# Optimization experiments

Hardware: AMD Instinct MI355X
Metric: run time of the kernel (lower is better)

The kernel has to match this reference:

```python
import jax, jax.numpy as jnp
import numpy as np

D = 2048
H = 16
HD = D // H
B = 2
T = 2048
EPS = 1e-6


def setup_inputs() -> dict:
    key = jax.random.key(0)
    ks = jax.random.split(key, 12)
    s = lambda fan_in: 1.0 / np.sqrt(fan_in)
    inp = {
        "x": jax.random.normal(ks[0], (B, T, D), dtype=jnp.float32),
        "mask": jnp.tril(jnp.ones((T, T), dtype=jnp.int32))[None, None],  # [1,1,T,T] causal
        "w_norm1": jnp.ones((D,), dtype=jnp.float32),
        "w_qkv": jax.random.normal(ks[1], (D, 3 * D), dtype=jnp.float32) * s(D),
        "b_qkv": jnp.zeros((3 * D,), dtype=jnp.float32),
        "w_proj": jax.random.normal(ks[2], (D, D), dtype=jnp.float32) * s(D),
        "b_proj": jnp.zeros((D,), dtype=jnp.float32),
        "w_norm2": jnp.ones((D,), dtype=jnp.float32),
        "w_fc1": jax.random.normal(ks[3], (D, 4 * D), dtype=jnp.float32) * s(D),
        "b_fc1": jnp.zeros((4 * D,), dtype=jnp.float32),
        "w_fc2": jax.random.normal(ks[4], (4 * D, D), dtype=jnp.float32) * s(4 * D),
        "b_fc2": jnpp_zeros((D,)) if False else jnp.zeros((D,), dtype=jnp.float32),
    }
    return inp


def _rmsnorm(x, w):
    # n = ||x||_2 / sqrt(d); out = x / (n + eps) * w  (matches source exactly)
    n = jnp.sqrt(jnp.sum(x * x, axis=-1, keepdims=True)) * (x.shape[-1] ** -0.5)
    return x / (n + EPS) * w


def _rope(q, k):
    # q,k: [B,H,T,HD]; half-split (non-interleaved) RoPE
    half = HD // 2
    idx = jnp.arange(half, dtype=jnp.float32)
    pos = jnp.arange(T, dtype=jnp.float32)[:, None]
    rates = jnp.power(10000.0, -2.0 * idx / HD)
    theta = pos * rates  # [T, half]
    cos, sin = jnp.cos(theta), jnp.sin(theta)

    def apply(x):
        x1, x2 = x[..., :half], x[..., half:]
        return jnp.concatenate([x1 * cos - x2 * sin, x1 * sin + x2 * cos], axis=-1)

    return apply(q), apply(k)


def reference(x, mask, w_norm1, w_qkv, b_qkv, w_proj, b_proj,
              w_norm2, w_fc1, b_fc1, w_fc2, b_fc2):
    # --- attention branch ---
    h = _rmsnorm(x, w_norm1)
    qkv = h @ w_qkv + b_qkv  # [B,T,3D]
    q, k, v = jnp.split(qkv, 3, axis=-1)
    q = q.reshape(B, T, H, HD).transpose(0, 2, 1, 3)
    k = k.reshape(B, T, H, HD).transpose(0, 2, 1, 3)
    v = v.reshape(B, T, H, HD).transpose(0, 2, 1, 3)
    q, k = _rope(q, k)
    att = jnp.einsum("bhqd,bhkd->bhqk", q, k) * (HD ** -0.5)
    att = jnp.where(mask == 0, -jnp.inf, att)
    att = jax.nn.softmax(att, axis=-1)
    y = jnp.einsum("bhqk,bhkd->bhqd", att, v)
    y = y.transpose(0, 2, 1, 3).reshape(B, T, D)
    x = x + (y @ w_proj + b_proj)
    # --- MLP branch ---
    h2 = _rmsnorm(x, w_norm2)
    h2 = jax.nn.silu(h2 @ w_fc1 + b_fc1)
    x = x + (h2 @ w_fc2 + b_fc2)
    return x
```

## Files before the change

### kernel.cpp

```cpp
#include <hip/hip_runtime.h>
#include <math.h>

typedef unsigned short u16;
typedef unsigned int u32;
typedef __attribute__((ext_vector_type(8))) short short8v;
typedef __attribute__((ext_vector_type(4))) float float4v;

#define T_SEQ 2048
#define D_MODEL 2048
#define N_HEADS 16
#define EPSV 1e-6f
#define MROWS 4096
#define MB (1024ull * 1024ull)

__device__ __forceinline__ u16 f2bf(float f) {
  union { float f; u32 u; } v; v.f = f;
  u32 r = v.u + 0x7fffu + ((v.u >> 16) & 1u);
  return (u16)(r >> 16);
}
__device__ __forceinline__ float bf2f(u16 h) {
  union { u32 u; float f; } v; v.u = ((u32)h) << 16;
  return v.f;
}
__device__ __forceinline__ void gl16(const void* g, void* l) {
  __builtin_amdgcn_global_load_lds(
      (const __attribute__((address_space(1))) void*)g,
      (__attribute__((address_space(3))) void*)l, 16, 0, 0);
}

__global__ __launch_bounds__(256) void rmsnorm_split_kernel(
    const float* __restrict__ x, const float* __restrict__ w,
    u16* __restrict__ oh, u16* __restrict__ ol) {
  const int row = blockIdx.x;
  const float* xr = x + (size_t)row * D_MODEL;

  float ss = 0.f;
#pragma unroll
  for (int it = 0; it < 2; ++it) {
    int i = threadIdx.x + it * 256;
    float4 v = ((const float4*)xr)[i];
    ss += v.x * v.x + v.y * v.y + v.z * v.z + v.w * v.w;
  }
#pragma unroll
  for (int off = 32; off >= 1; off >>= 1) ss += __shfl_xor(ss, off, 64);
  __shared__ float red[4];
  if ((threadIdx.x & 63) == 0) red[threadIdx.x >> 6] = ss;
  __syncthreads();
  const float tot = red[0] + red[1] + red[2] + red[3];
  const float n = sqrtf(tot) * 0.022097086912079608f;
  const float inv = 1.0f / (n + EPSV);

  u16* ohr = oh + (size_t)row * D_MODEL;
  u16* olr = ol + (size_t)row * D_MODEL;
#pragma unroll
  for (int it = 0; it < 2; ++it) {
    int i = threadIdx.x + it * 256;
    float4 v = ((const float4*)xr)[i];
    float4 wv = ((const float4*)w)[i];
    float o[4] = {v.x * inv * wv.x, v.y * inv * wv.y, v.z * inv * wv.z,
                  v.w * inv * wv.w};
    ushort4 h4, l4;
    h4.x = f2bf(o[0]); l4.x = f2bf(o[0] - bf2f(h4.x));
    h4.y = f2bf(o[1]); l4.y = f2bf(o[1] - bf2f(h4.y));
    h4.z = f2bf(o[2]); l4.z = f2bf(o[2] - bf2f(h4.z));
    h4.w = f2bf(o[3]); l4.w = f2bf(o[3] - bf2f(h4.w));
    ((ushort4*)ohr)[i] = h4;
    ((ushort4*)olr)[i] = l4;
  }
}

__global__ __launch_bounds__(256) void splitT_kernel(
    const float* __restrict__ W, u16* __restrict__ Th, u16* __restrict__ Tl,
    int K, int N) {
  __shared__ float tile[32][33];
  const int tx = threadIdx.x, ty = threadIdx.y;
  const int n0 = blockIdx.x * 32, k0 = blockIdx.y * 32;
#pragma unroll
  for (int i = 0; i < 4; ++i)
    tile[ty + i * 8][tx] = W[(size_t)(k0 + ty + i * 8) * N + n0 + tx];
  __syncthreads();
#pragma unroll
  for (int i = 0; i < 4; ++i) {
    const float v = tile[tx][ty + i * 8];
    const int n = n0 + ty + i * 8, k = k0 + tx;
    const u16 h = f2bf(v);
    Th[(size_t)n * K + k] = h;
    Tl[(size_t)n * K + k] = f2bf(v - bf2f(h));
  }
}

template <int OUT>
__global__ __launch_bounds__(512) void mgemm_kernel(
    const u16* __restrict__ Ah, const u16* __restrict__ Al,
    const u16* __restrict__ Bh, const u16* __restrict__ Bl,
    const float* __restrict__ bias, const float* __restrict__ res,
    float* __restrict__ C, u16* __restrict__ Ch, u16* __restrict__ Cl,
    int N, int K) {
  __shared__ __align__(16) u16 lds[2][24576];

  const int tid = threadIdx.x;
  const int lane = tid & 63;
  const int wv = tid >> 6;
  const int wr = wv >> 1, wc = wv & 1;

  const int gx = N >> 7;
  const int nwg = gx << 4;
  int id = blockIdx.x;
  id = (id & 7) * (nwg >> 3) + (id >> 3);
  const int g = id >> 6, w = id & 63;
  const int bn = (g << 2) + (w & 3);
  const int bm = w >> 2;

  const int ls = lane >> 3;
  const int ss = (lane & 7) ^ ls;
  const int sel = ss >> 2;
  const int sc = (ss & 3) << 3;

  const u16* aS[4];
  const u16* bS[2];
#pragma unroll
  for (int cc = 0; cc < 4; ++cc)
    aS[cc] = (sel ? Al : Ah) +
             (size_t)(bm * 256 + wv * 32 + cc * 8 + ls) * K + sc;
#pragma unroll
  for (int cc = 0; cc < 2; ++cc)
    bS[cc] = (sel ? Bl : Bh) +
             (size_t)(bn * 128 + wv * 16 + cc * 8 + ls) * K + sc;

  const int S = K >> 5;

  float4v acc[4][4];
  const float4v zf = {0.f, 0.f, 0.f, 0.f};
#pragma unroll
  for (int i = 0; i < 4; ++i)
#pragma unroll
    for (int j = 0; j < 4; ++j) acc[i][j] = zf;

  auto STAGE = [&](int buf, int step) {
    const int kk = step << 5;
    char* lb = (char*)&lds[buf][0];
#pragma unroll
    for (int cc = 0; cc < 4; ++cc)
      gl16(aS[cc] + kk, lb + (wv * 4 + cc) * 1024);
#pragma unroll
    for (int cc = 0; cc < 2; ++cc)
      gl16(bS[cc] + kk, lb + 32768 + (wv * 2 + cc) * 1024);
  };

  const int l15 = lane & 15;
  const int kq = lane >> 4;
  const int swz = (l15 & 7) << 4;
  const int hOff = (kq * 16) ^ swz;
  const int lOff = (64 + kq * 16) ^ swz;
  int aRow[4], bRow[4];
#pragma unroll
  for (int mi = 0; mi < 4; ++mi) aRow[mi] = (wr * 64 + mi * 16 + l15) * 128;
#pragma unroll
  for (int ni = 0; ni < 4; ++ni)
    bRow[ni] = 32768 + (wc * 64 + ni * 16 + l15) * 128;

  auto COMPUTE = [&](int buf) {
    const char* lb = (const char*)&lds[buf][0];
    short8v bh[4], bl[4];
#pragma unroll
    for (int ni = 0; ni < 4; ++ni) {
      bh[ni] = *(const short8v*)(lb + bRow[ni] + hOff);
      bl[ni] = *(const short8v*)(lb + bRow[ni] + lOff);
    }
    short8v ah[4], al[4];
#pragma unroll
    for (int mi = 0; mi < 4; ++mi) {
      ah[mi] = *(const short8v*)(lb + aRow[mi] + hOff);
      al[mi] = *(const short8v*)(lb + aRow[mi] + lOff);
    }
    __builtin_amdgcn_s_setprio(1);
#pragma unroll
    for (int mi = 0; mi < 4; ++mi) {
#pragma unroll
      for (int ni = 0; ni < 4; ++ni) {
        acc[mi][ni] = __builtin_amdgcn_mfma_f32_16x16x32_bf16(
            ah[mi], bh[ni], acc[mi][ni], 0, 0, 0);
        acc[mi][ni] = __builtin_amdgcn_mfma_f32_16x16x32_bf16(
            al[mi], bh[ni], acc[mi][ni], 0, 0, 0);
        acc[mi][ni] = __builtin_amdgcn_mfma_f32_16x16x32_bf16(
            ah[mi], bl[ni], acc[mi][ni], 0, 0, 0);
      }
    }
    __builtin_amdgcn_s_setprio(0);
  };

  STAGE(0, 0);
  int t = 0;
  for (; t < S - 1; ++t) {
    STAGE((t + 1) & 1, t + 1);
    asm volatile("s_waitcnt vmcnt(6)" ::: "memory");
    __builtin_amdgcn_s_barrier();
    __builtin_amdgcn_sched_barrier(0);
    COMPUTE(t & 1);
    __builtin_amdgcn_s_barrier();
  }
  asm volatile("s_waitcnt vmcnt(0)" ::: "memory");
  __builtin_amdgcn_s_barrier();
  __builtin_amdgcn_sched_barrier(0);
  COMPUTE(t & 1);

  const int rsub = kq * 4;
#pragma unroll
  for (int mi = 0; mi < 4; ++mi) {
#pragma unroll
    for (int ni = 0; ni < 4; ++ni) {
      const int col = bn * 128 + wc * 64 + ni * 16 + l15;
      const float bb = bias[col];
      const float4v v = acc[mi][ni];
#pragma unroll
      for (int r = 0; r < 4; ++r) {
        const int row = bm * 256 + wr * 64 + mi * 16 + rsub + r;
        float val = v[r] + bb;
        if (OUT == 1) val += res[(size_t)row * N + col];
        if (OUT == 2) {
          const float sv = val / (1.f + expf(-val));
          const u16 hh = f2bf(sv);
          Ch[(size_t)row * N + col] = hh;
          Cl[(size_t)row * N + col] = f2bf(sv - bf2f(hh));
        } else {
          C[(size_t)row * N + col] = val;
        }
      }
    }
  }
}

__global__ __launch_bounds__(256) void rope_table_kernel(
    float* __restrict__ ct, float* __restrict__ st) {
  const int p = blockIdx.x * 256 + threadIdx.x;
  const int i = p & 63;
  const int t = p >> 6;
  const float ratef = (float)pow(10000.0, -(double)i / 64.0);
  const float theta = (float)t * ratef;
  ct[p] = (float)cos((double)theta);
  st[p] = (float)sin((double)theta);
}

__global__ __launch_bounds__(256) void rope_split_kernel(
    const float* __restrict__ qkv, const float* __restrict__ ct,
    const float* __restrict__ st, u16* __restrict__ Qh, u16* __restrict__ Ql,
    u16* __restrict__ Kh, u16* __restrict__ Kl, u16* __restrict__ Vth,
    u16* __restrict__ Vtl) {
  const int tt = blockIdx.x, bh = blockIdx.y;
  const int b = bh >> 4, h = bh & 15;
  const int tid = threadIdx.x;
  const int tl = tid >> 2, quad = tid & 3;
  const int t = tt * 64 + tl;
  const size_t rowbase = ((size_t)(b * T_SEQ + t)) * 6144 + h * 128;
  const size_t qkbase = (size_t)bh * T_SEQ * 128 + (size_t)t * 128;

#pragma unroll
  for (int i = 0; i < 4; ++i) {
    const int d0 = quad * 4 + i * 16;
    const float4 c4 = *(const float4*)&ct[(size_t)t * 64 + d0];
    const float4 s4 = *(const float4*)&st[(size_t)t * 64 + d0];
#pragma unroll
    for (int qk = 0; qk < 2; ++qk) {
      const size_t src = rowbase + qk * D_MODEL + d0;
      const float4 a = *(const float4*)&qkv[src];
      const float4 bb = *(const float4*)&qkv[src + 64];
      float o1[4] = {a.x * c4.x - bb.x * s4.x, a.y * c4.y - bb.y * s4.y,
                     a.z * c4.z - bb.z * s4.z, a.w * c4.w - bb.w * s4.w};
      float o2[4] = {a.x * s4.x + bb.x * c4.x, a.y * s4.y + bb.y * c4.y,
                     a.z * s4.z + bb.z * c4.z, a.w * s4.w + bb.w * c4.w};
      u16* dh = (qk == 0) ? Qh : Kh;
      u16* dl = (qk == 0) ? Ql : Kl;
      ushort4 h4, l4;
      h4.x = f2bf(o1[0]); l4.x = f2bf(o1[0] - bf2f(h4.x));
      h4.y = f2bf(o1[1]); l4.y = f2bf(o1[1] - bf2f(h4.y));
      h4.z = f2bf(o1[2]); l4.z = f2bf(o1[2] - bf2f(h4.z));
      h4.w = f2bf(o1[3]); l4.w = f2bf(o1[3] - bf2f(h4.w));
      *(ushort4*)&dh[qkbase + d0] = h4;
      *(ushort4*)&dl[qkbase + d0] = l4;
      h4.x = f2bf(o2[0]); l4.x = f2bf(o2[0] - bf2f(h4.x));
      h4.y = f2bf(o2[1]); l4.y = f2bf(o2[1] - bf2f(h4.y));
      h4.z = f2bf(o2[2]); l4.z = f2bf(o2[2] - bf2f(h4.z));
      h4.w = f2bf(o2[3]); l4.w = f2bf(o2[3] - bf2f(h4.w));
      *(ushort4*)&dh[qkbase + 64 + d0] = h4;
      *(ushort4*)&dl[qkbase + 64 + d0] = l4;
    }
  }

  __shared__ float Lv[64][132];
#pragma unroll
  for (int i = 0; i < 8; ++i) {
    const int c0 = quad * 4 + i * 16;
    const float4 v = *(const float4*)&qkv[rowbase + 2 * D_MODEL + c0];
    *(float4*)&Lv[tl][c0] = v;
  }
  __syncthreads();
  const int dd = tid >> 1, half = tid & 1;
  const size_t vtb =
      (size_t)bh * 128 * T_SEQ + (size_t)dd * T_SEQ + tt * 64 + half * 32;
#pragma unroll
  for (int g = 0; g < 4; ++g) {
    short8v hv, lv;
#pragma unroll
    for (int e = 0; e < 8; ++e) {
      const float v = Lv[half * 32 + g * 8 + e][dd];
      const u16 hh = f2bf(v);
      hv[e] = (short)hh;
      lv[e] = (short)f2bf(v - bf2f(hh));
    }
    *(short8v*)&Vth[vtb + g * 8] = hv;
    *(short8v*)&Vtl[vtb + g * 8] = lv;
  }
}

__global__ __launch_bounds__(256) void attn_mfma_kernel(
    const u16* __restrict__ Qh, const u16* __restrict__ Ql,
    const u16* __restrict__ Kh, const u16* __restrict__ Kl,
    const u16* __restrict__ Vth, const u16* __restrict__ Vtl,
    u16* __restrict__ yh, u16* __restrict__ yl) {
  __shared__ __align__(16) u16 lds[4][8192];
  int id = blockIdx.x;
  id = (id & 7) * 128 + (id >> 3);
  const int qt = id & 31, bh = id >> 5;
  const int tid = threadIdx.x, lane = tid & 63, wv = tid >> 6;
  const int l15 = lane & 15, kq = lane >> 4;

  const size_t hQK = (size_t)bh * T_SEQ * 128;
  const size_t hVt = (size_t)bh * 128 * T_SEQ;

  short8v qfh[4], qfl[4];
  {
    const size_t qb = hQK + (size_t)(qt * 64 + wv * 16 + l15) * 128 + kq * 8;
#pragma unroll
    for (int ks = 0; ks < 4; ++ks) {
      qfh[ks] = *(const short8v*)(Qh + qb + ks * 32);
      qfl[ks] = *(const short8v*)(Ql + qb + ks * 32);
    }
  }

  const float4v zf = {0.f, 0.f, 0.f, 0.f};
  float4v Oa[8];
#pragma unroll
  for (int i = 0; i < 8; ++i) Oa[i] = zf;
  float mM = -INFINITY, lS = 0.f;

  for (int kt = 0; kt <= qt; ++kt) {
    __syncthreads();
    if (wv < 2) {
      const u16* src = (wv == 0 ? Kh : Kl) + hQK + (size_t)kt * 64 * 128;
#pragma unroll
      for (int i = 0; i < 16; ++i) {
        const int off = i * 1024 + lane * 16;
        const int soff = off ^ (((off >> 8) & 7) << 4);
        gl16((const char*)src + soff, (char*)(&lds[wv][0]) + i * 1024);
      }
    } else {
      const u16* src = (wv == 2 ? Vth : Vtl) + hVt + (size_t)kt * 64;
#pragma unroll
      for (int i = 0; i < 16; ++i) {
        const int off = i * 1024 + lane * 16;
        const int d = off >> 7;
        const int soff = (off & 127) ^ ((d & 7) << 4);
        gl16((const char*)src + (size_t)d * 4096 + soff,
             (char*)(&lds[wv][0]) + i * 1024);
      }
    }
    __syncthreads();

    float4v sa[4];
#pragma unroll
    for (int i = 0; i < 4; ++i) sa[i] = zf;
#pragma unroll
    for (int ks = 0; ks < 4; ++ks) {
#pragma unroll
      for (int mf = 0; mf < 4; ++mf) {
        const int ro =
            ((mf * 16 + l15) * 256 + ks * 64 + kq * 16) ^ ((l15 & 7) << 4);
        const short8v kh = *(const short8v*)((const char*)(&lds[0][0]) + ro);
        const short8v kl = *(const short8v*)((const char*)(&lds[1][0]) + ro);
        sa[mf] = __builtin_amdgcn_mfma_f32_16x16x32_bf16(kh, qfh[ks], sa[mf], 0, 0, 0);
        sa[mf] = __builtin_amdgcn_mfma_f32_16x16x32_bf16(kl, qfh[ks], sa[mf], 0, 0, 0);
        sa[mf] = __builtin_amdgcn_mfma_f32_16x16x32_bf16(kh, qfl[ks], sa[mf], 0, 0, 0);
      }
    }

    const float scale = 0.08838834764831845f;
    const int qloc = wv * 16 + l15;
    float p[4][4];
    float pmax = -INFINITY;
#pragma unroll
    for (int mf = 0; mf < 4; ++mf)
#pragma unroll
      for (int r = 0; r < 4; ++r) {
        float v = sa[mf][r] * scale;
        if (kt == qt && (mf * 16 + kq * 4 + r) > qloc) v = -1e30f;
        p[mf][r] = v;
        pmax = fmaxf(pmax, v);
      }
    pmax = fmaxf(pmax, __shfl_xor(pmax, 16, 64));
    pmax = fmaxf(pmax, __shfl_xor(pmax, 32, 64));
    const float mnew = fmaxf(mM, pmax);
    const float alpha = __expf(mM - mnew);
    float rs = 0.f;
#pragma unroll
    for (int mf = 0; mf < 4; ++mf)
#pragma unroll
      for (int r = 0; r < 4; ++r) {
        const float pv = __expf(p[mf][r] - mnew);
        p[mf][r] = pv;
        rs += pv;
      }
    rs += __shfl_xor(rs, 16, 64);
    rs += __shfl_xor(rs, 32, 64);
    lS = lS * alpha + rs;
    mM = mnew;

    const int abase = (lane & 48) + ((lane >> 4) << 2);
    float al4[4];
#pragma unroll
    for (int r = 0; r < 4; ++r) al4[r] = __shfl(alpha, abase + r, 64);
#pragma unroll
    for (int nf = 0; nf < 8; ++nf)
#pragma unroll
      for (int r = 0; r < 4; ++r) Oa[nf][r] *= al4[r];

    short8v pah[2], pal[2];
#pragma unroll
    for (int ks2 = 0; ks2 < 2; ++ks2) {
#pragma unroll
      for (int j = 0; j < 8; ++j) {
        const int src = ((lane >> 4) & 1) * 32 + (j >> 2) * 16 + l15;
        const float va = __shfl(p[2 * ks2][j & 3], src, 64);
        const float vb = __shfl(p[2 * ks2 + 1][j & 3], src, 64);
        const float pj = (lane >= 32) ? vb : va;
        const u16 hh = f2bf(pj);
        pah[ks2][j] = (short)hh;
        pal[ks2][j] = (short)f2bf(pj - bf2f(hh));
      }
    }

#pragma unroll
    for (int nf = 0; nf < 8; ++nf) {
#pragma unroll
      for (int ks2 = 0; ks2 < 2; ++ks2) {
        const int ro =
            ((nf * 16 + l15) * 128 + ks2 * 64 + kq * 16) ^ ((l15 & 7) << 4);
        const short8v vh = *(const short8v*)((const char*)(&lds[2][0]) + ro);
        const short8v vl = *(const short8v*)((const char*)(&lds[3][0]) + ro);
        Oa[nf] = __builtin_amdgcn_mfma_f32_16x16x32_bf16(pah[ks2], vh, Oa[nf], 0, 0, 0);
        Oa[nf] = __builtin_amdgcn_mfma_f32_16x16x32_bf16(pal[ks2], vh, Oa[nf], 0, 0, 0);
        Oa[nf] = __builtin_amdgcn_mfma_f32_16x16x32_bf16(pah[ks2], vl, Oa[nf], 0, 0, 0);
      }
    }
  }

  const int abase = (lane & 48) + ((lane >> 4) << 2);
  float li[4];
#pragma unroll
  for (int r = 0; r < 4; ++r) li[r] = 1.f / __shfl(lS, abase + r, 64);
  const int b = bh >> 4, h = bh & 15;
#pragma unroll
  for (int r = 0; r < 4; ++r) {
    const int t = qt * 64 + wv * 16 + kq * 4 + r;
    const size_t ob = ((size_t)(b * T_SEQ + t)) * D_MODEL + h * 128 + l15;
#pragma unroll
    for (int nf = 0; nf < 8; ++nf) {
      const float val = Oa[nf][r] * li[r];
      const u16 hh = f2bf(val);
      yh[ob + nf * 16] = hh;
      yl[ob + nf * 16] = f2bf(val - bf2f(hh));
    }
  }
}

extern "C" void kernel_launch(void* const* d_in, const int* in_sizes, int n_in,
                              void* d_out, int out_size, void* d_ws,
                              size_t ws_size, hipStream_t stream) {
  const float* x       = (const float*)d_in[0];
  const float* w_norm1 = (const float*)d_in[2];
  const float* w_qkv   = (const float*)d_in[3];
  const float* b_qkv   = (const float*)d_in[4];
  const float* w_proj  = (const float*)d_in[5];
  const float* b_proj  = (const float*)d_in[6];
  const float* w_norm2 = (const float*)d_in[7];
  const float* w_fc1   = (const float*)d_in[8];
  const float* b_fc1   = (const float*)d_in[9];
  const float* w_fc2   = (const float*)d_in[10];
  const float* b_fc2   = (const float*)d_in[11];
  float* out = (float*)d_out;

  char* wsb = (char*)d_ws;
  float* qkvb = (float*)wsb;
  u16* fc1h = (u16*)wsb;
  u16* fc1l = (u16*)(wsb + 64 * MB);
  u16* qsh = (u16*)(wsb + 96 * MB);
  u16* qsl = (u16*)(wsb + 112 * MB);
  u16* ksh = (u16*)(wsb + 128 * MB);
  u16* ksl = (u16*)(wsb + 144 * MB);
  u16* vth = (u16*)(wsb + 160 * MB);
  u16* vtl = (u16*)(wsb + 176 * MB);
  u16* wth_qkv = (u16*)(wsb + 96 * MB);
  u16* wtl_qkv = (u16*)(wsb + 120 * MB);
  u16* wth_p = (u16*)(wsb + 96 * MB);
  u16* wtl_p = (u16*)(wsb + 104 * MB);
  u16* wth_f = (u16*)(wsb + 128 * MB);
  u16* wtl_f = (u16*)(wsb + 160 * MB);
  u16* ah = (u16*)(wsb + 192 * MB);
  u16* al = (u16*)(wsb + 208 * MB);
  u16* yh = ah;
  u16* yl = al;
  float* ct = (float*)(wsb + 224 * MB);
  float* st = ct + 131072;

  rope_table_kernel<<<512, 256, 0, stream>>>(ct, st);

  rmsnorm_split_kernel<<<4096, 256, 0, stream>>>(x, w_norm1, ah, al);
  splitT_kernel<<<dim3(192, 64), dim3(32, 8), 0, stream>>>(w_qkv, wth_qkv,
                                                           wtl_qkv, 2048, 6144);
  mgemm_kernel<0><<<dim3(48 * 16), 512, 0, stream>>>(
      ah, al, wth_qkv, wtl_qkv, b_qkv, nullptr, qkvb, nullptr, nullptr, 6144,
      2048);
  rope_split_kernel<<<dim3(32, 32), 256, 0, stream>>>(qkvb, ct, st, qsh, qsl,
                                                      ksh, ksl, vth, vtl);
  attn_mfma_kernel<<<dim3(1024), 256, 0, stream>>>(qsh, qsl, ksh, ksl, vth,
                                                   vtl, yh, yl);
  splitT_kernel<<<dim3(64, 64), dim3(32, 8), 0, stream>>>(w_proj, wth_p, wtl_p,
                                                          2048, 2048);
  mgemm_kernel<1><<<dim3(16 * 16), 512, 0, stream>>>(
      yh, yl, wth_p, wtl_p, b_proj, x, out, nullptr, nullptr, 2048, 2048);
  rmsnorm_split_kernel<<<4096, 256, 0, stream>>>(out, w_norm2, ah, al);
  splitT_kernel<<<dim3(256, 64), dim3(32, 8), 0, stream>>>(w_fc1, wth_f, wtl_f,
                                                           2048, 8192);
  mgemm_kernel<2><<<dim3(64 * 16), 512, 0, stream>>>(
      ah, al, wth_f, wtl_f, b_fc1, nullptr, nullptr, fc1h, fc1l, 8192, 2048);
  splitT_kernel<<<dim3(64, 256), dim3(32, 8), 0, stream>>>(w_fc2, wth_f, wtl_f,
                                                           8192, 2048);
  mgemm_kernel<1><<<dim3(16 * 16), 512, 0, stream>>>(
      fc1h, fc1l, wth_f, wtl_f, b_fc2, out, out, nullptr, nullptr, 2048, 8192);
}
```

Measured before the change: 1.669 ms.

## Interleave global prefetch and LDS reads with MFMA phases in GEMM main loop

Replaces the stage-then-compute double-buffer loop with a finer-grained schedule. The next tile's A and B global-to-LDS copies are issued in pieces between MFMA groups, and B fragments are read one column group at a time. The aim is to overlap memory traffic with matrix-core work and lower register pressure from holding all B fragments. It adds several workgroup barriers per K step, which may cost synchronization overhead.

Result: no change. 1.642 ms (-1.6%).

```diff
diff --git a/kernel.cpp b/kernel.cpp
--- a/kernel.cpp
+++ b/kernel.cpp
@@ -136,17 +136,6 @@
 #pragma unroll
     for (int j = 0; j < 4; ++j) acc[i][j] = zf;
 
-  auto STAGE = [&](int buf, int step) {
-    const int kk = step << 5;
-    char* lb = (char*)&lds[buf][0];
-#pragma unroll
-    for (int cc = 0; cc < 4; ++cc)
-      gl16(aS[cc] + kk, lb + (wv * 4 + cc) * 1024);
-#pragma unroll
-    for (int cc = 0; cc < 2; ++cc)
-      gl16(bS[cc] + kk, lb + 32768 + (wv * 2 + cc) * 1024);
-  };
-
   const int l15 = lane & 15;
   const int kq = lane >> 4;
   const int swz = (l15 & 7) << 4;
@@ -159,50 +148,85 @@
   for (int ni = 0; ni < 4; ++ni)
     bRow[ni] = 32768 + (wc * 64 + ni * 16 + l15) * 128;
 
-  auto COMPUTE = [&](int buf) {
-    const char* lb = (const char*)&lds[buf][0];
-    short8v bh[4], bl[4];
-#pragma unroll
-    for (int ni = 0; ni < 4; ++ni) {
-      bh[ni] = *(const short8v*)(lb + bRow[ni] + hOff);
-      bl[ni] = *(const short8v*)(lb + bRow[ni] + lOff);
-    }
+  {
+    char* lb = (char*)&lds[0][0];
+#pragma unroll
+    for (int cc = 0; cc < 4; ++cc) gl16(aS[cc], lb + (wv * 4 + cc) * 1024);
+#pragma unroll
+    for (int cc = 0; cc < 2; ++cc)
+      gl16(bS[cc], lb + 32768 + (wv * 2 + cc) * 1024);
+  }
+
+  for (int t = 0; t < S; ++t) {
+    const int c = t & 1;
+    const char* lb = (const char*)&lds[c][0];
+    char* sb = (char*)&lds[c ^ 1][0];
+    const bool pre = (t + 1 < S);
+    const int kk = (t + 1) << 5;
+
+    if (pre) {
+      gl16(aS[0] + kk, sb + (wv * 4 + 0) * 1024);
+      gl16(aS[1] + kk, sb + (wv * 4 + 1) * 1024);
+      asm volatile("s_waitcnt vmcnt(2)" ::: "memory");
+    } else {
+      asm volatile("s_waitcnt vmcnt(0)" ::: "memory");
+    }
+    __builtin_amdgcn_s_barrier();
+    __builtin_amdgcn_sched_barrier(0);
+
     short8v ah[4], al[4];
 #pragma unroll
     for (int mi = 0; mi < 4; ++mi) {
       ah[mi] = *(const short8v*)(lb + aRow[mi] + hOff);
       al[mi] = *(const short8v*)(lb + aRow[mi] + lOff);
     }
-    __builtin_amdgcn_s_setprio(1);
-#pragma unroll
-    for (int mi = 0; mi < 4; ++mi) {
-#pragma unroll
-      for (int ni = 0; ni < 4; ++ni) {
-        acc[mi][ni] = __builtin_amdgcn_mfma_f32_16x16x32_bf16(
-            ah[mi], bh[ni], acc[mi][ni], 0, 0, 0);
-        acc[mi][ni] = __builtin_amdgcn_mfma_f32_16x16x32_bf16(
-            al[mi], bh[ni], acc[mi][ni], 0, 0, 0);
-        acc[mi][ni] = __builtin_amdgcn_mfma_f32_16x16x32_bf16(
-            ah[mi], bl[ni], acc[mi][ni], 0, 0, 0);
-      }
-    }
-    __builtin_amdgcn_s_setprio(0);
-  };
-
-  STAGE(0, 0);
-  int t = 0;
-  for (; t < S - 1; ++t) {
-    STAGE((t + 1) & 1, t + 1);
-    asm volatile("s_waitcnt vmcnt(6)" ::: "memory");
+    short8v bh = *(const short8v*)(lb + bRow[0] + hOff);
+    short8v bl = *(const short8v*)(lb + bRow[0] + lOff);
+    if (pre) {
+      gl16(aS[2] + kk, sb + (wv * 4 + 2) * 1024);
+      gl16(aS[3] + kk, sb + (wv * 4 + 3) * 1024);
+    }
     __builtin_amdgcn_s_barrier();
     __builtin_amdgcn_sched_barrier(0);
-    COMPUTE(t & 1);
+    __builtin_amdgcn_s_setprio(1);
+#pragma unroll
+    for (int mi = 0; mi < 4; ++mi) {
+      acc[mi][0] = __builtin_amdgcn_mfma_f32_16x16x32_bf16(ah[mi], bh,
+                                                           acc[mi][0], 0, 0, 0);
+      acc[mi][0] = __builtin_amdgcn_mfma_f32_16x16x32_bf16(al[mi], bh,
+                                                           acc[mi][0], 0, 0, 0);
+      acc[mi][0] = __builtin_amdgcn_mfma_f32_16x16x32_bf16(ah[mi], bl,
+                                                           acc[mi][0], 0, 0, 0);
+    }
+    __builtin_amdgcn_s_setprio(0);
     __builtin_amdgcn_s_barrier();
-  }
-  asm volatile("s_waitcnt vmcnt(0)" ::: "memory");
-  __builtin_amdgcn_s_barrier();
-  __builtin_amdgcn_sched_barrier(0);
-  COMPUTE(t & 1);
+    __builtin_amdgcn_sched_barrier(0);
+
+#pragma unroll
+    for (int ni = 1; ni < 4; ++ni) {
+      bh = *(const short8v*)(lb + bRow[ni] + hOff);
+      bl = *(const short8v*)(lb + bRow[ni] + lOff);
+      if (ni == 1 && pre) {
+        gl16(bS[0] + kk, sb + 32768 + (wv * 2 + 0) * 1024);
+        gl16(bS[1] + kk, sb + 32768 + (wv * 2 + 1) * 1024);
+      }
+      __builtin_amdgcn_s_barrier();
+      __builtin_amdgcn_sched_barrier(0);
+      __builtin_amdgcn_s_setprio(1);
+#pragma unroll
+      for (int mi = 0; mi < 4; ++mi) {
+        acc[mi][ni] = __builtin_amdgcn_mfma_f32_16x16x32_bf16(
+            ah[mi], bh, acc[mi][ni], 0, 0, 0);
+        acc[mi][ni] = __builtin_amdgcn_mfma_f32_16x16x32_bf16(
+            al[mi], bh, acc[mi][ni], 0, 0, 0);
+        acc[mi][ni] = __builtin_amdgcn_mfma_f32_16x16x32_bf16(
+            ah[mi], bl, acc[mi][ni], 0, 0, 0);
+      }
+      __builtin_amdgcn_s_setprio(0);
+      __builtin_amdgcn_s_barrier();
+      __builtin_amdgcn_sched_barrier(0);
+    }
+  }
 
   const int rsub = kq * 4;
 #pragma unroll
```
